# Performance work log

Hardware: AMD Instinct MI355X
Metric: run time of the kernel (lower is better)

Reference implementation:

```python
import jax, jax.numpy as jnp
import numpy as np

N = 100000
E = 1600000
EPS = 1e-5  # BatchNorm eps


def setup_inputs() -> dict:
    key = jax.random.key(0)
    ks = jax.random.split(key, 8)
    x = jax.random.normal(ks[0], (N, 8), jnp.float32)
    edge_index = jax.random.randint(ks[1], (2, E), 0, N, dtype=jnp.int64)

    def lin(k, i, o):
        return jax.random.normal(k, (i, o), jnp.float32) / np.float32(np.sqrt(i))

    d = {
        'x': x, 'edge_index': edge_index,
        'W1': lin(ks[2], 8, 64),  'b1': jnp.zeros((64,), jnp.float32),
        'g1': jnp.ones((64,), jnp.float32), 'be1': jnp.zeros((64,), jnp.float32),
        'rm1': jnp.zeros((64,), jnp.float32), 'rv1': jnp.ones((64,), jnp.float32),
        'W2': lin(ks[3], 64, 64), 'b2': jnp.zeros((64,), jnp.float32),
        'g2': jnp.ones((64,), jnp.float32), 'be2': jnp.zeros((64,), jnp.float32),
        'rm2': jnp.zeros((64,), jnp.float32), 'rv2': jnp.ones((64,), jnp.float32),
        'W3': lin(ks[4], 64, 32), 'b3': jnp.zeros((32,), jnp.float32),
        'g3': jnp.ones((32,), jnp.float32), 'be3': jnp.zeros((32,), jnp.float32),
        'rm3': jnp.zeros((32,), jnp.float32), 'rv3': jnp.ones((32,), jnp.float32),
        'Wc': lin(ks[5], 32, 2),  'bc': jnp.zeros((2,), jnp.float32),
    }
    return d


def _gcn_conv(x, W, b, src, dst):
    # PyG GCNConv (improved=False): add self-loops with weight 1, symmetric norm.
    h = x @ W                                               # [N, out]
    deg = jax.ops.segment_sum(jnp.ones((E,), x.dtype), dst, num_segments=N) + 1.0
    dinv = jax.lax.rsqrt(deg)                               # deg >= 1 (self loop)
    norm = dinv[src] * dinv[dst]                            # [E]
    agg = jax.ops.segment_sum(h[src] * norm[:, None], dst, num_segments=N)
    agg = agg + h * (dinv * dinv)[:, None]                  # self-loop messages
    return agg + b


def _bn_eval(x, g, be, rm, rv):
    return (x - rm) * jax.lax.rsqrt(rv + EPS) * g + be


def reference(x, edge_index,
              W1, b1, g1, be1, rm1, rv1,
              W2, b2, g2, be2, rm2, rv2,
              W3, b3, g3, be3, rm3, rv3,
              Wc, bc):
    src, dst = edge_index[0], edge_index[1]
    h = jax.nn.relu(_bn_eval(_gcn_conv(x, W1, b1, src, dst), g1, be1, rm1, rv1))
    h = jax.nn.relu(_bn_eval(_gcn_conv(h, W2, b2, src, dst), g2, be2, rm2, rv2))
    h = jax.nn.relu(_bn_eval(_gcn_conv(h, W3, b3, src, dst), g3, be3, rm3, rv3))
    logits = h @ Wc + bc                                    # [N, 2]
    return jax.nn.log_softmax(logits, axis=-1)
```

## Files before the change

### kernel.cpp

```cpp
#include <hip/hip_runtime.h>
#include <hip/hip_fp16.h>

#define BN_EPS 1e-5f
#define BCAP 5120
#define EDCAP_H64 768
#define EDCAP_CLS 1280

__device__ __forceinline__ unsigned f2u(float a, float b) {
  __half2 h = __floats2half2_rn(a, b);
  return *reinterpret_cast<unsigned*>(&h);
}
__device__ __forceinline__ __half2 uh2(unsigned u) {
  return *reinterpret_cast<__half2*>(&u);
}
__device__ __forceinline__ float2 h22f2(__half2 h) { return __half22float2(h); }
__device__ __forceinline__ __half2 h2shfl_xor(__half2 v, int m) {
  int i = *reinterpret_cast<int*>(&v);
  i = __shfl_xor(i, m);
  return *reinterpret_cast<__half2*>(&i);
}

__global__ void prep(const float* __restrict__ b1, const float* __restrict__ g1,
                     const float* __restrict__ be1, const float* __restrict__ rm1,
                     const float* __restrict__ rv1,
                     const float* __restrict__ b2, const float* __restrict__ g2,
                     const float* __restrict__ be2, const float* __restrict__ rm2,
                     const float* __restrict__ rv2,
                     const float* __restrict__ b3, const float* __restrict__ g3,
                     const float* __restrict__ be3, const float* __restrict__ rm3,
                     const float* __restrict__ rv3,
                     float* __restrict__ bn, int* __restrict__ bcur, int NB) {
  if (blockIdx.x == 0) {
    const int t = threadIdx.x;
    if (t < 64) {
      const float s = g1[t] * rsqrtf(rv1[t] + BN_EPS);
      bn[t] = s;
      bn[64 + t] = (b1[t] - rm1[t]) * s + be1[t];
    } else if (t < 128) {
      const int c = t - 64;
      const float s = g2[c] * rsqrtf(rv2[c] + BN_EPS);
      bn[128 + c] = s;
      bn[192 + c] = (b2[c] - rm2[c]) * s + be2[c];
    } else if (t < 160) {
      const int c = t - 128;
      const float s = g3[c] * rsqrtf(rv3[c] + BN_EPS);
      bn[256 + c] = s;
      bn[288 + c] = (b3[c] - rm3[c]) * s + be3[c];
    }
  } else {
    const int i = (blockIdx.x - 1) * 256 + threadIdx.x;
    if (i <= NB) bcur[i] = 0;
  }
}

__global__ void p1_partition(const int* __restrict__ ei, int* __restrict__ bucketbuf,
                             int* __restrict__ bcur, int E_, int NB) {
  __shared__ int pk[4096];
  __shared__ short bk[4096];
  __shared__ int hist[512];
  __shared__ int bbase[512];
  const int tid = threadIdx.x;
  const int e0 = blockIdx.x * 4096;
  const int ecount = min(4096, E_ - e0);
  for (int i = tid; i < NB; i += 256) hist[i] = 0;
  __syncthreads();
  for (int i = tid; i < ecount; i += 256) {
    const int s = ei[e0 + i];
    const int d = ei[(size_t)E_ + e0 + i];
    pk[i] = ((d & 255) << 24) | s;
    const int b = d >> 8;
    bk[i] = (short)b;
    atomicAdd(&hist[b], 1);
  }
  __syncthreads();
  for (int i = tid; i < NB; i += 256) {
    const int c = hist[i];
    bbase[i] = c ? atomicAdd(&bcur[i], c) : 0;
    hist[i] = 0;
  }
  __syncthreads();
  for (int i = tid; i < ecount; i += 256) {
    const int b = bk[i];
    const int slot = bbase[b] + atomicAdd(&hist[b], 1);
    bucketbuf[(size_t)b * BCAP + slot] = pk[i];
  }
}

__global__ void p2_sort(const int* __restrict__ bucketbuf, const int* __restrict__ bcur,
                        int* __restrict__ gcursor, int* __restrict__ edata,
                        int* __restrict__ rbeg, int* __restrict__ rend,
                        float* __restrict__ dinv, const float* __restrict__ x,
                        __half2* __restrict__ xs, int N_) {
  __shared__ int cntl[256];
  __shared__ int scn[256];
  __shared__ int cur[256];
  __shared__ float dinvl[256];
  __shared__ int sbuf[BCAP];
  __shared__ int sbase;
  const int b = blockIdx.x;
  const int tid = threadIdx.x;
  const int m = bcur[b];
  const int* srcp = bucketbuf + (size_t)b * BCAP;
  cntl[tid] = 0;
  __syncthreads();
  for (int i = tid; i < m; i += 256) atomicAdd(&cntl[(unsigned)srcp[i] >> 24], 1);
  __syncthreads();
  if (tid == 0) sbase = atomicAdd(gcursor, m);
  const int cnt = cntl[tid];
  scn[tid] = cnt;
  __syncthreads();
  for (int off = 1; off < 256; off <<= 1) {
    int u = (tid >= off) ? scn[tid - off] : 0;
    __syncthreads();
    scn[tid] += u;
    __syncthreads();
  }
  const int excl = scn[tid] - cnt;
  cur[tid] = excl;
  const int base = sbase;
  const int node = (b << 8) + tid;
  const float dn = rsqrtf((float)cnt + 1.0f);
  dinvl[tid] = dn;
  if (node < N_) {
    rbeg[node] = base + excl;
    rend[node] = base + excl + cnt;
    dinv[node] = dn;
  }
  __syncthreads();
  for (int i = tid; i < m; i += 256) {
    const int v = srcp[i];
    const int slot = atomicAdd(&cur[(unsigned)v >> 24], 1);
    sbuf[slot] = v & 0xFFFFFF;
  }
  __syncthreads();
  for (int i = tid; i < m; i += 256) edata[(size_t)base + i] = sbuf[i];
  const int nb0 = b << 8;
  for (int i = tid; i < 1024; i += 256) {
    const int nd = nb0 + (i >> 2);
    if (nd < N_) {
      const float d2 = dinvl[i >> 2];
      const float2 v2 = reinterpret_cast<const float2*>(x)[(size_t)nd * 4 + (i & 3)];
      xs[(size_t)nd * 4 + (i & 3)] = __floats2half2_rn(v2.x * d2, v2.y * d2);
    }
  }
}

__global__ void gx_mm1(const __half* __restrict__ xs, const float* __restrict__ dinv,
                       const int* __restrict__ rbeg, const int* __restrict__ rend,
                       const int* __restrict__ edata, const float* __restrict__ W1,
                       const float* __restrict__ bn, __half* __restrict__ t1, int n) {
  __shared__ float shagg[32][8];
  __shared__ float shw[8 * 64];
  const int tid = threadIdx.x;
  for (int i = tid; i < 512; i += 256) shw[i] = W1[i];
  const int node0 = blockIdx.x * 32;
  const int lane = tid & 63;
  const int nl = ((tid >> 6) << 3) + (lane >> 3);
  const int grp = lane & 7;
  const int node = node0 + nl;
  if (node < n) {
    const int beg = rbeg[node], end = rend[node];
    const uint4* xv = reinterpret_cast<const uint4*>(xs);
    __half2 c0 = __half2{0, 0}, c1 = c0, c2 = c0, c3 = c0;
    int e = beg + grp;
    for (; e + 8 < end; e += 16) {
      const uint4 q0 = xv[edata[e]];
      const uint4 q1 = xv[edata[e + 8]];
      c0 = __hadd2(c0, uh2(q0.x)); c1 = __hadd2(c1, uh2(q0.y));
      c2 = __hadd2(c2, uh2(q0.z)); c3 = __hadd2(c3, uh2(q0.w));
      c0 = __hadd2(c0, uh2(q1.x)); c1 = __hadd2(c1, uh2(q1.y));
      c2 = __hadd2(c2, uh2(q1.z)); c3 = __hadd2(c3, uh2(q1.w));
    }
    if (e < end) {
      const uint4 q = xv[edata[e]];
      c0 = __hadd2(c0, uh2(q.x)); c1 = __hadd2(c1, uh2(q.y));
      c2 = __hadd2(c2, uh2(q.z)); c3 = __hadd2(c3, uh2(q.w));
    }
#pragma unroll
    for (int m = 1; m <= 4; m <<= 1) {
      c0 = __hadd2(c0, h2shfl_xor(c0, m));
      c1 = __hadd2(c1, h2shfl_xor(c1, m));
      c2 = __hadd2(c2, h2shfl_xor(c2, m));
      c3 = __hadd2(c3, h2shfl_xor(c3, m));
    }
    if (grp == 0) {
      const uint4 q = xv[node];
      c0 = __hadd2(c0, uh2(q.x)); c1 = __hadd2(c1, uh2(q.y));
      c2 = __hadd2(c2, uh2(q.z)); c3 = __hadd2(c3, uh2(q.w));
      const float dn = dinv[node];
      const float2 f0 = h22f2(c0), f1 = h22f2(c1);
      const float2 f2 = h22f2(c2), f3 = h22f2(c3);
      shagg[nl][0] = f0.x * dn; shagg[nl][1] = f0.y * dn;
      shagg[nl][2] = f1.x * dn; shagg[nl][3] = f1.y * dn;
      shagg[nl][4] = f2.x * dn; shagg[nl][5] = f2.y * dn;
      shagg[nl][6] = f3.x * dn; shagg[nl][7] = f3.y * dn;
    }
  }
  __syncthreads();
  const int mn = tid >> 3;
  const int node2 = node0 + mn;
  if (node2 >= n) return;
  const int c = (tid & 7) * 8;
  float a[8] = {0, 0, 0, 0, 0, 0, 0, 0};
#pragma unroll
  for (int k = 0; k < 8; ++k) {
    const float s = shagg[mn][k];
#pragma unroll
    for (int j = 0; j < 8; ++j) a[j] += s * shw[k * 64 + c + j];
  }
  float v[8];
#pragma unroll
  for (int j = 0; j < 8; ++j) {
    float t = a[j] * bn[c + j] + bn[64 + c + j];
    v[j] = t > 0.0f ? t : 0.0f;
  }
  uint4 o;
  o.x = f2u(v[0], v[1]);
  o.y = f2u(v[2], v[3]);
  o.z = f2u(v[4], v[5]);
  o.w = f2u(v[6], v[7]);
  reinterpret_cast<uint4*>(t1)[(size_t)node2 * 8 + (tid & 7)] = o;
}

__global__ void mm2(const __half* __restrict__ t1, const float* __restrict__ W2,
                    const float* __restrict__ dinv, __half* __restrict__ h2, int n) {
  __shared__ __half2 shin[64 * 33];
  __shared__ uint4 shw[32 * 16];
  const int tid = threadIdx.x;
  const int node0 = blockIdx.x * 64;
  const __half2* t1h = reinterpret_cast<const __half2*>(t1);
  for (int i = tid; i < 64 * 32; i += 256) {
    const int nd = i >> 5, kp = i & 31;
    __half2 v = __half2{0, 0};
    if (node0 + nd < n) v = t1h[(size_t)(node0 + nd) * 32 + kp];
    shin[nd * 33 + kp] = v;
  }
  __half2* shwh = reinterpret_cast<__half2*>(shw);
  for (int i = tid; i < 32 * 64; i += 256) {
    const int kp = i >> 6, c = i & 63;
    shwh[kp * 64 + c] = __floats2half2_rn(W2[(2 * kp) * 64 + c], W2[(2 * kp + 1) * 64 + c]);
  }
  __syncthreads();

  const int cq = tid & 15;
  const int nb = (tid >> 4) * 4;
  float acc[4][4];
#pragma unroll
  for (int j = 0; j < 4; ++j)
#pragma unroll
    for (int k = 0; k < 4; ++k) acc[j][k] = 0.0f;

  for (int kp = 0; kp < 32; ++kp) {
    const uint4 wq = shw[kp * 16 + cq];
    const float2 w0 = h22f2(uh2(wq.x)), w1 = h22f2(uh2(wq.y));
    const float2 w2 = h22f2(uh2(wq.z)), w3 = h22f2(uh2(wq.w));
#pragma unroll
    for (int j = 0; j < 4; ++j) {
      const float2 s = h22f2(shin[(nb + j) * 33 + kp]);
      acc[j][0] += s.x * w0.x + s.y * w0.y;
      acc[j][1] += s.x * w1.x + s.y * w1.y;
      acc[j][2] += s.x * w2.x + s.y * w2.y;
      acc[j][3] += s.x * w3.x + s.y * w3.y;
    }
  }
#pragma unroll
  for (int j = 0; j < 4; ++j) {
    const int node = node0 + nb + j;
    if (node < n) {
      const float dn = dinv[node];
      uint2 o;
      o.x = f2u(acc[j][0] * dn, acc[j][1] * dn);
      o.y = f2u(acc[j][2] * dn, acc[j][3] * dn);
      reinterpret_cast<uint2*>(h2)[(size_t)node * 16 + cq] = o;
    }
  }
}

__global__ void gather_h64(const __half* __restrict__ h, const float* __restrict__ dinv,
                           const int* __restrict__ rbeg, const int* __restrict__ rend,
                           const int* __restrict__ edata, __half* __restrict__ agg, int n) {
  __shared__ int se[EDCAP_H64];
  const int tid = threadIdx.x;
  const int node0 = blockIdx.x * 8;
  const int last = min(node0 + 7, n - 1);
  const int gb = rbeg[node0];
  const int total = rend[last] - gb;
  const bool lds = (total <= EDCAP_H64);
  if (lds) {
    for (int i = tid; i < total; i += 256) se[i] = edata[gb + i];
  }
  __syncthreads();
  const int lane = tid & 63;
  const int node = node0 + ((tid >> 6) << 1) + (lane >> 5);
  if (node >= n) return;
  const int sub = lane & 31;
  const int qi = sub & 7;
  const int grp = sub >> 3;
  const uint4* hv = reinterpret_cast<const uint4*>(h);
  __half2 c0 = __half2{0, 0}, c1 = c0, c2 = c0, c3 = c0;
  if (lds) {
    const int beg = rbeg[node] - gb, end = rend[node] - gb;
    int e = beg + grp;
    for (; e + 12 < end; e += 16) {
      const int s0 = se[e], s1 = se[e + 4], s2 = se[e + 8], s3 = se[e + 12];
      const uint4 q0 = hv[(size_t)s0 * 8 + qi];
      const uint4 q1 = hv[(size_t)s1 * 8 + qi];
      const uint4 q2 = hv[(size_t)s2 * 8 + qi];
      const uint4 q3 = hv[(size_t)s3 * 8 + qi];
      c0 = __hadd2(c0, uh2(q0.x)); c1 = __hadd2(c1, uh2(q0.y));
      c2 = __hadd2(c2, uh2(q0.z)); c3 = __hadd2(c3, uh2(q0.w));
      c0 = __hadd2(c0, uh2(q1.x)); c1 = __hadd2(c1, uh2(q1.y));
      c2 = __hadd2(c2, uh2(q1.z)); c3 = __hadd2(c3, uh2(q1.w));
      c0 = __hadd2(c0, uh2(q2.x)); c1 = __hadd2(c1, uh2(q2.y));
      c2 = __hadd2(c2, uh2(q2.z)); c3 = __hadd2(c3, uh2(q2.w));
      c0 = __hadd2(c0, uh2(q3.x)); c1 = __hadd2(c1, uh2(q3.y));
      c2 = __hadd2(c2, uh2(q3.z)); c3 = __hadd2(c3, uh2(q3.w));
    }
    for (; e < end; e += 4) {
      const uint4 q = hv[(size_t)se[e] * 8 + qi];
      c0 = __hadd2(c0, uh2(q.x)); c1 = __hadd2(c1, uh2(q.y));
      c2 = __hadd2(c2, uh2(q.z)); c3 = __hadd2(c3, uh2(q.w));
    }
  } else {
    const int beg = rbeg[node], end = rend[node];
    int e = beg + grp;
    for (; e + 12 < end; e += 16) {
      const int s0 = edata[e], s1 = edata[e + 4], s2 = edata[e + 8], s3 = edata[e + 12];
      const uint4 q0 = hv[(size_t)s0 * 8 + qi];
      const uint4 q1 = hv[(size_t)s1 * 8 + qi];
      const uint4 q2 = hv[(size_t)s2 * 8 + qi];
      const uint4 q3 = hv[(size_t)s3 * 8 + qi];
      c0 = __hadd2(c0, uh2(q0.x)); c1 = __hadd2(c1, uh2(q0.y));
      c2 = __hadd2(c2, uh2(q0.z)); c3 = __hadd2(c3, uh2(q0.w));
      c0 = __hadd2(c0, uh2(q1.x)); c1 = __hadd2(c1, uh2(q1.y));
      c2 = __hadd2(c2, uh2(q1.z)); c3 = __hadd2(c3, uh2(q1.w));
      c0 = __hadd2(c0, uh2(q2.x)); c1 = __hadd2(c1, uh2(q2.y));
      c2 = __hadd2(c2, uh2(q2.z)); c3 = __hadd2(c3, uh2(q2.w));
      c0 = __hadd2(c0, uh2(q3.x)); c1 = __hadd2(c1, uh2(q3.y));
      c2 = __hadd2(c2, uh2(q3.z)); c3 = __hadd2(c3, uh2(q3.w));
    }
    for (; e < end; e += 4) {
      const uint4 q = hv[(size_t)edata[e] * 8 + qi];
      c0 = __hadd2(c0, uh2(q.x)); c1 = __hadd2(c1, uh2(q.y));
      c2 = __hadd2(c2, uh2(q.z)); c3 = __hadd2(c3, uh2(q.w));
    }
  }
#pragma unroll
  for (int m = 8; m <= 16; m <<= 1) {
    c0 = __hadd2(c0, h2shfl_xor(c0, m));
    c1 = __hadd2(c1, h2shfl_xor(c1, m));
    c2 = __hadd2(c2, h2shfl_xor(c2, m));
    c3 = __hadd2(c3, h2shfl_xor(c3, m));
  }
  if (grp == 0) {
    const uint4 q = hv[(size_t)node * 8 + qi];
    c0 = __hadd2(c0, uh2(q.x)); c1 = __hadd2(c1, uh2(q.y));
    c2 = __hadd2(c2, uh2(q.z)); c3 = __hadd2(c3, uh2(q.w));
    const float dn = dinv[node];
    const float2 f0 = h22f2(c0), f1 = h22f2(c1);
    const float2 f2 = h22f2(c2), f3 = h22f2(c3);
    uint4 o;
    o.x = f2u(f0.x * dn, f0.y * dn);
    o.y = f2u(f1.x * dn, f1.y * dn);
    o.z = f2u(f2.x * dn, f2.y * dn);
    o.w = f2u(f3.x * dn, f3.y * dn);
    reinterpret_cast<uint4*>(agg)[(size_t)node * 8 + qi] = o;
  }
}

__global__ void mm3_act(const __half* __restrict__ agg2, const float* __restrict__ W3,
                        const float* __restrict__ bn, const float* __restrict__ dinv,
                        __half* __restrict__ h3, int n) {
  __shared__ __half2 shin[128 * 33];
  __shared__ uint4 shw[32 * 8];
  const int tid = threadIdx.x;
  const int node0 = blockIdx.x * 128;
  const __half2* ah = reinterpret_cast<const __half2*>(agg2);
  for (int i = tid; i < 128 * 32; i += 256) {
    const int nd = i >> 5, kp = i & 31;
    __half2 o = __half2{0, 0};
    if (node0 + nd < n) {
      const float2 v = h22f2(ah[(size_t)(node0 + nd) * 32 + kp]);
      float v0 = v.x * bn[128 + 2 * kp] + bn[192 + 2 * kp];
      float v1 = v.y * bn[128 + 2 * kp + 1] + bn[192 + 2 * kp + 1];
      v0 = v0 > 0.0f ? v0 : 0.0f;
      v1 = v1 > 0.0f ? v1 : 0.0f;
      o = __floats2half2_rn(v0, v1);
    }
    shin[nd * 33 + kp] = o;
  }
  __half2* shwh = reinterpret_cast<__half2*>(shw);
  for (int i = tid; i < 32 * 32; i += 256) {
    const int kp = i >> 5, c = i & 31;
    shwh[kp * 32 + c] = __floats2half2_rn(W3[(2 * kp) * 32 + c], W3[(2 * kp + 1) * 32 + c]);
  }
  __syncthreads();

  const int cq = tid & 7;
  const int nb = (tid >> 3) * 4;
  float acc[4][4];
#pragma unroll
  for (int j = 0; j < 4; ++j)
#pragma unroll
    for (int k = 0; k < 4; ++k) acc[j][k] = 0.0f;

  for (int kp = 0; kp < 32; ++kp) {
    const uint4 wq = shw[kp * 8 + cq];
    const float2 w0 = h22f2(uh2(wq.x)), w1 = h22f2(uh2(wq.y));
    const float2 w2 = h22f2(uh2(wq.z)), w3 = h22f2(uh2(wq.w));
#pragma unroll
    for (int j = 0; j < 4; ++j) {
      const float2 s = h22f2(shin[(nb + j) * 33 + kp]);
      acc[j][0] += s.x * w0.x + s.y * w0.y;
      acc[j][1] += s.x * w1.x + s.y * w1.y;
      acc[j][2] += s.x * w2.x + s.y * w2.y;
      acc[j][3] += s.x * w3.x + s.y * w3.y;
    }
  }
#pragma unroll
  for (int j = 0; j < 4; ++j) {
    const int node = node0 + nb + j;
    if (node < n) {
      const float dn = dinv[node];
      uint2 o;
      o.x = f2u(acc[j][0] * dn, acc[j][1] * dn);
      o.y = f2u(acc[j][2] * dn, acc[j][3] * dn);
      reinterpret_cast<uint2*>(h3)[(size_t)node * 8 + cq] = o;
    }
  }
}

__global__ void gather_cls(const __half* __restrict__ h, const float* __restrict__ dinv,
                           const int* __restrict__ rbeg, const int* __restrict__ rend,
                           const int* __restrict__ edata, const float* __restrict__ bn,
                           const float* __restrict__ Wc, const float* __restrict__ bc,
                           float* __restrict__ out, int n) {
  __shared__ int se[EDCAP_CLS];
  const int tid = threadIdx.x;
  const int node0 = blockIdx.x * 16;
  const int last = min(node0 + 15, n - 1);
  const int gb = rbeg[node0];
  const int total = rend[last] - gb;
  const bool lds = (total <= EDCAP_CLS);
  if (lds) {
    for (int i = tid; i < total; i += 256) se[i] = edata[gb + i];
  }
  __syncthreads();
  const int lane = tid & 63;
  const int node = node0 + ((tid >> 6) << 2) + (lane >> 4);
  if (node >= n) return;
  const int qi = lane & 3;
  const int grp = (lane >> 2) & 3;
  const uint4* hv = reinterpret_cast<const uint4*>(h);
  __half2 c0 = __half2{0, 0}, c1 = c0, c2 = c0, c3 = c0;
  if (lds) {
    const int beg = rbeg[node] - gb, end = rend[node] - gb;
    int e = beg + grp;
    for (; e + 12 < end; e += 16) {
      const int s0 = se[e], s1 = se[e + 4], s2 = se[e + 8], s3 = se[e + 12];
      const uint4 q0 = hv[(size_t)s0 * 4 + qi];
      const uint4 q1 = hv[(size_t)s1 * 4 + qi];
      const uint4 q2 = hv[(size_t)s2 * 4 + qi];
      const uint4 q3 = hv[(size_t)s3 * 4 + qi];
      c0 = __hadd2(c0, uh2(q0.x)); c1 = __hadd2(c1, uh2(q0.y));
      c2 = __hadd2(c2, uh2(q0.z)); c3 = __hadd2(c3, uh2(q0.w));
      c0 = __hadd2(c0, uh2(q1.x)); c1 = __hadd2(c1, uh2(q1.y));
      c2 = __hadd2(c2, uh2(q1.z)); c3 = __hadd2(c3, uh2(q1.w));
      c0 = __hadd2(c0, uh2(q2.x)); c1 = __hadd2(c1, uh2(q2.y));
      c2 = __hadd2(c2, uh2(q2.z)); c3 = __hadd2(c3, uh2(q2.w));
      c0 = __hadd2(c0, uh2(q3.x)); c1 = __hadd2(c1, uh2(q3.y));
      c2 = __hadd2(c2, uh2(q3.z)); c3 = __hadd2(c3, uh2(q3.w));
    }
    for (; e < end; e += 4) {
      const uint4 q = hv[(size_t)se[e] * 4 + qi];
      c0 = __hadd2(c0, uh2(q.x)); c1 = __hadd2(c1, uh2(q.y));
      c2 = __hadd2(c2, uh2(q.z)); c3 = __hadd2(c3, uh2(q.w));
    }
  } else {
    const int beg = rbeg[node], end = rend[node];
    int e = beg + grp;
    for (; e + 12 < end; e += 16) {
      const int s0 = edata[e], s1 = edata[e + 4], s2 = edata[e + 8], s3 = edata[e + 12];
      const uint4 q0 = hv[(size_t)s0 * 4 + qi];
      const uint4 q1 = hv[(size_t)s1 * 4 + qi];
      const uint4 q2 = hv[(size_t)s2 * 4 + qi];
      const uint4 q3 = hv[(size_t)s3 * 4 + qi];
      c0 = __hadd2(c0, uh2(q0.x)); c1 = __hadd2(c1, uh2(q0.y));
      c2 = __hadd2(c2, uh2(q0.z)); c3 = __hadd2(c3, uh2(q0.w));
      c0 = __hadd2(c0, uh2(q1.x)); c1 = __hadd2(c1, uh2(q1.y));
      c2 = __hadd2(c2, uh2(q1.z)); c3 = __hadd2(c3, uh2(q1.w));
      c0 = __hadd2(c0, uh2(q2.x)); c1 = __hadd2(c1, uh2(q2.y));
      c2 = __hadd2(c2, uh2(q2.z)); c3 = __hadd2(c3, uh2(q2.w));
      c0 = __hadd2(c0, uh2(q3.x)); c1 = __hadd2(c1, uh2(q3.y));
      c2 = __hadd2(c2, uh2(q3.z)); c3 = __hadd2(c3, uh2(q3.w));
    }
    for (; e < end; e += 4) {
      const uint4 q = hv[(size_t)edata[e] * 4 + qi];
      c0 = __hadd2(c0, uh2(q.x)); c1 = __hadd2(c1, uh2(q.y));
      c2 = __hadd2(c2, uh2(q.z)); c3 = __hadd2(c3, uh2(q.w));
    }
  }
#pragma unroll
  for (int m = 4; m <= 8; m <<= 1) {
    c0 = __hadd2(c0, h2shfl_xor(c0, m));
    c1 = __hadd2(c1, h2shfl_xor(c1, m));
    c2 = __hadd2(c2, h2shfl_xor(c2, m));
    c3 = __hadd2(c3, h2shfl_xor(c3, m));
  }
  if (grp != 0) return;
  {
    const uint4 q = hv[(size_t)node * 4 + qi];
    c0 = __hadd2(c0, uh2(q.x)); c1 = __hadd2(c1, uh2(q.y));
    c2 = __hadd2(c2, uh2(q.z)); c3 = __hadd2(c3, uh2(q.w));
  }
  const float dn = dinv[node];
  const float2 f0 = h22f2(c0), f1 = h22f2(c1);
  const float2 f2 = h22f2(c2), f3 = h22f2(c3);
  const float v[8] = {f0.x * dn, f0.y * dn, f1.x * dn, f1.y * dn,
                      f2.x * dn, f2.y * dn, f3.x * dn, f3.y * dn};
  float l0 = 0.0f, l1 = 0.0f;
#pragma unroll
  for (int j = 0; j < 8; ++j) {
    const int c = qi * 8 + j;
    float t = v[j] * bn[256 + c] + bn[288 + c];
    t = t > 0.0f ? t : 0.0f;
    const float2 w = *reinterpret_cast<const float2*>(&Wc[c * 2]);
    l0 += t * w.x;
    l1 += t * w.y;
  }
  l0 += __shfl_xor(l0, 1); l1 += __shfl_xor(l1, 1);
  l0 += __shfl_xor(l0, 2); l1 += __shfl_xor(l1, 2);
  if (qi == 0) {
    l0 += bc[0];
    l1 += bc[1];
    const float m = fmaxf(l0, l1);
    const float lse = m + log1pf(expf(-fabsf(l0 - l1)));
    *reinterpret_cast<float2*>(&out[(size_t)node * 2]) = make_float2(l0 - lse, l1 - lse);
  }
}

extern "C" void kernel_launch(void* const* d_in, const int* in_sizes, int n_in,
                              void* d_out, int out_size, void* d_ws, size_t ws_size,
                              hipStream_t stream) {
  const float* x  = (const float*)d_in[0];
  const int* ei   = (const int*)d_in[1];
  const float* W1 = (const float*)d_in[2];
  const float* b1 = (const float*)d_in[3];
  const float* g1 = (const float*)d_in[4];
  const float* be1 = (const float*)d_in[5];
  const float* rm1 = (const float*)d_in[6];
  const float* rv1 = (const float*)d_in[7];
  const float* W2 = (const float*)d_in[8];
  const float* b2 = (const float*)d_in[9];
  const float* g2 = (const float*)d_in[10];
  const float* be2 = (const float*)d_in[11];
  const float* rm2 = (const float*)d_in[12];
  const float* rv2 = (const float*)d_in[13];
  const float* W3 = (const float*)d_in[14];
  const float* b3 = (const float*)d_in[15];
  const float* g3 = (const float*)d_in[16];
  const float* be3 = (const float*)d_in[17];
  const float* rm3 = (const float*)d_in[18];
  const float* rv3 = (const float*)d_in[19];
  const float* Wc = (const float*)d_in[20];
  const float* bc = (const float*)d_in[21];

  const int N_ = in_sizes[0] / 8;
  const int E_ = in_sizes[1] / 2;
  const int NB = (N_ + 255) >> 8;

  auto align = [](size_t v) { return (v + 255) & ~(size_t)255; };
  char* ws = (char*)d_ws;
  size_t off = 0;
  float* dinv   = (float*)(ws + off); off += align((size_t)N_ * 4);
  int* bcur     = (int*)(ws + off);   off += align(((size_t)NB + 1) * 4);
  int* rbeg     = (int*)(ws + off);   off += align((size_t)N_ * 4);
  int* rend     = (int*)(ws + off);   off += align((size_t)N_ * 4);
  float* bnbuf  = (float*)(ws + off); off += align(320 * 4);
  int* edata    = (int*)(ws + off);   off += align((size_t)E_ * 4);
  __half* xs    = (__half*)(ws + off); off += align((size_t)N_ * 8 * 2);
  char* regionA = ws + off;           off += align((size_t)N_ * 64 * 2);
  char* regionB = ws + off;           off += align((size_t)N_ * 64 * 2);

  int* bucketbuf = (int*)regionA;
  __half* t1   = (__half*)regionA;
  __half* agg2 = (__half*)regionA;
  __half* h2   = (__half*)regionB;
  __half* h3   = (__half*)regionB;
  int* gcursor = bcur + NB;

  prep<<<1 + (NB + 1 + 255) / 256, 256, 0, stream>>>(b1, g1, be1, rm1, rv1,
                                                     b2, g2, be2, rm2, rv2,
                                                     b3, g3, be3, rm3, rv3, bnbuf, bcur, NB);
  p1_partition<<<(E_ + 4095) / 4096, 256, 0, stream>>>(ei, bucketbuf, bcur, E_, NB);
  p2_sort<<<NB, 256, 0, stream>>>(bucketbuf, bcur, gcursor, edata, rbeg, rend,
                                  dinv, x, (__half2*)xs, N_);

  gx_mm1<<<(N_ + 31) / 32, 256, 0, stream>>>(xs, dinv, rbeg, rend, edata, W1, bnbuf, t1, N_);

  mm2<<<(N_ + 63) / 64, 256, 0, stream>>>(t1, W2, dinv, h2, N_);
  gather_h64<<<(N_ + 7) / 8, 256, 0, stream>>>(h2, dinv, rbeg, rend, edata, agg2, N_);

  mm3_act<<<(N_ + 127) / 128, 256, 0, stream>>>(agg2, W3, bnbuf, dinv, h3, N_);
  gather_cls<<<(N_ + 15) / 16, 256, 0, stream>>>(h3, dinv, rbeg, rend, edata,
                                                 bnbuf, Wc, bc, (float*)d_out, N_);
}
```

Before: 166.7 us.

## Fuse layer-1 aggregate with both dense matmuls and gather with mm3

Merges gx_mm1 and mm2 into one kernel that keeps the layer-1 activations in LDS and applies W2 directly. It also merges the layer-2 gather with BN/ReLU and the W3 matmul, so the 64-wide intermediate t1 and agg2 never go to global memory. This removes two kernel launches and two full N×64 half-precision round-trips. The cost is higher LDS use per block and W2/W3 staging repeated in every small block, especially in gh64_mm3 with only 8 nodes per block.

```diff
diff --git a/kernel.cpp b/kernel.cpp
--- a/kernel.cpp
+++ b/kernel.cpp
@@ -145,15 +145,25 @@
   }
 }
 
-__global__ void gx_mm1(const __half* __restrict__ xs, const float* __restrict__ dinv,
-                       const int* __restrict__ rbeg, const int* __restrict__ rend,
-                       const int* __restrict__ edata, const float* __restrict__ W1,
-                       const float* __restrict__ bn, __half* __restrict__ t1, int n) {
+__global__ void l12(const __half* __restrict__ xs, const float* __restrict__ dinv,
+                    const int* __restrict__ rbeg, const int* __restrict__ rend,
+                    const int* __restrict__ edata, const float* __restrict__ W1,
+                    const float* __restrict__ W2, const float* __restrict__ bn,
+                    __half* __restrict__ h2, int n) {
+  __shared__ float shw1[8 * 64];
   __shared__ float shagg[32][8];
-  __shared__ float shw[8 * 64];
+  __shared__ __half2 sht1[32 * 33];
+  __shared__ uint4 shw2[32 * 16];
   const int tid = threadIdx.x;
-  for (int i = tid; i < 512; i += 256) shw[i] = W1[i];
   const int node0 = blockIdx.x * 32;
+  for (int i = tid; i < 512; i += 256) shw1[i] = W1[i];
+  {
+    __half2* shw2h = reinterpret_cast<__half2*>(shw2);
+    for (int i = tid; i < 32 * 64; i += 256) {
+      const int kp = i >> 6, c = i & 63;
+      shw2h[kp * 64 + c] = __floats2half2_rn(W2[(2 * kp) * 64 + c], W2[(2 * kp + 1) * 64 + c]);
+    }
+  }
   const int lane = tid & 63;
   const int nl = ((tid >> 6) << 3) + (lane >> 3);
   const int grp = lane & 7;
@@ -197,66 +207,43 @@
     }
   }
   __syncthreads();
-  const int mn = tid >> 3;
-  const int node2 = node0 + mn;
-  if (node2 >= n) return;
-  const int c = (tid & 7) * 8;
-  float a[8] = {0, 0, 0, 0, 0, 0, 0, 0};
-#pragma unroll
-  for (int k = 0; k < 8; ++k) {
-    const float s = shagg[mn][k];
-#pragma unroll
-    for (int j = 0; j < 8; ++j) a[j] += s * shw[k * 64 + c + j];
-  }
-  float v[8];
-#pragma unroll
-  for (int j = 0; j < 8; ++j) {
-    float t = a[j] * bn[c + j] + bn[64 + c + j];
-    v[j] = t > 0.0f ? t : 0.0f;
-  }
-  uint4 o;
-  o.x = f2u(v[0], v[1]);
-  o.y = f2u(v[2], v[3]);
-  o.z = f2u(v[4], v[5]);
-  o.w = f2u(v[6], v[7]);
-  reinterpret_cast<uint4*>(t1)[(size_t)node2 * 8 + (tid & 7)] = o;
-}
-
-__global__ void mm2(const __half* __restrict__ t1, const float* __restrict__ W2,
-                    const float* __restrict__ dinv, __half* __restrict__ h2, int n) {
-  __shared__ __half2 shin[64 * 33];
-  __shared__ uint4 shw[32 * 16];
-  const int tid = threadIdx.x;
-  const int node0 = blockIdx.x * 64;
-  const __half2* t1h = reinterpret_cast<const __half2*>(t1);
-  for (int i = tid; i < 64 * 32; i += 256) {
-    const int nd = i >> 5, kp = i & 31;
-    __half2 v = __half2{0, 0};
-    if (node0 + nd < n) v = t1h[(size_t)(node0 + nd) * 32 + kp];
-    shin[nd * 33 + kp] = v;
-  }
-  __half2* shwh = reinterpret_cast<__half2*>(shw);
-  for (int i = tid; i < 32 * 64; i += 256) {
-    const int kp = i >> 6, c = i & 63;
-    shwh[kp * 64 + c] = __floats2half2_rn(W2[(2 * kp) * 64 + c], W2[(2 * kp + 1) * 64 + c]);
-  }
-  __syncthreads();
-
+  {
+    const int mn = tid >> 3;
+    const int c = (tid & 7) * 8;
+    if (node0 + mn < n) {
+      float a[8] = {0, 0, 0, 0, 0, 0, 0, 0};
+#pragma unroll
+      for (int k = 0; k < 8; ++k) {
+        const float s = shagg[mn][k];
+#pragma unroll
+        for (int j = 0; j < 8; ++j) a[j] += s * shw1[k * 64 + c + j];
+      }
+      float v[8];
+#pragma unroll
+      for (int j = 0; j < 8; ++j) {
+        float t = a[j] * bn[c + j] + bn[64 + c + j];
+        v[j] = t > 0.0f ? t : 0.0f;
+      }
+#pragma unroll
+      for (int j = 0; j < 4; ++j)
+        sht1[mn * 33 + (tid & 7) * 4 + j] = __floats2half2_rn(v[2 * j], v[2 * j + 1]);
+    }
+  }
+  __syncthreads();
   const int cq = tid & 15;
-  const int nb = (tid >> 4) * 4;
-  float acc[4][4];
-#pragma unroll
-  for (int j = 0; j < 4; ++j)
+  const int nbs = (tid >> 4) * 2;
+  float acc[2][4];
+#pragma unroll
+  for (int j = 0; j < 2; ++j)
 #pragma unroll
     for (int k = 0; k < 4; ++k) acc[j][k] = 0.0f;
-
   for (int kp = 0; kp < 32; ++kp) {
-    const uint4 wq = shw[kp * 16 + cq];
+    const uint4 wq = shw2[kp * 16 + cq];
     const float2 w0 = h22f2(uh2(wq.x)), w1 = h22f2(uh2(wq.y));
     const float2 w2 = h22f2(uh2(wq.z)), w3 = h22f2(uh2(wq.w));
 #pragma unroll
-    for (int j = 0; j < 4; ++j) {
-      const float2 s = h22f2(shin[(nb + j) * 33 + kp]);
+    for (int j = 0; j < 2; ++j) {
+      const float2 s = h22f2(sht1[(nbs + j) * 33 + kp]);
       acc[j][0] += s.x * w0.x + s.y * w0.y;
       acc[j][1] += s.x * w1.x + s.y * w1.y;
       acc[j][2] += s.x * w2.x + s.y * w2.y;
@@ -264,22 +251,26 @@
     }
   }
 #pragma unroll
-  for (int j = 0; j < 4; ++j) {
-    const int node = node0 + nb + j;
-    if (node < n) {
-      const float dn = dinv[node];
+  for (int j = 0; j < 2; ++j) {
+    const int nd = node0 + nbs + j;
+    if (nd < n) {
+      const float dn = dinv[nd];
       uint2 o;
       o.x = f2u(acc[j][0] * dn, acc[j][1] * dn);
       o.y = f2u(acc[j][2] * dn, acc[j][3] * dn);
-      reinterpret_cast<uint2*>(h2)[(size_t)node * 16 + cq] = o;
-    }
-  }
-}
-
-__global__ void gather_h64(const __half* __restrict__ h, const float* __restrict__ dinv,
-                           const int* __restrict__ rbeg, const int* __restrict__ rend,
-                           const int* __restrict__ edata, __half* __restrict__ agg, int n) {
+      reinterpret_cast<uint2*>(h2)[(size_t)nd * 16 + cq] = o;
+    }
+  }
+}
+
+__global__ void gh64_mm3(const __half* __restrict__ h, const float* __restrict__ dinv,
+                         const int* __restrict__ rbeg, const int* __restrict__ rend,
+                         const int* __restrict__ edata, const float* __restrict__ W3,
+                         const float* __restrict__ bn, __half* __restrict__ h3, int n) {
   __shared__ int se[EDCAP_H64];
+  __shared__ __half2 shagg2[8 * 33];
+  __shared__ __half2 shw3[32 * 32];
+  __shared__ float shbn[128];
   const int tid = threadIdx.x;
   const int node0 = blockIdx.x * 8;
   const int last = min(node0 + 7, n - 1);
@@ -289,144 +280,107 @@
   if (lds) {
     for (int i = tid; i < total; i += 256) se[i] = edata[gb + i];
   }
+  for (int i = tid; i < 32 * 32; i += 256) {
+    const int kp = i >> 5, c = i & 31;
+    shw3[kp * 32 + c] = __floats2half2_rn(W3[(2 * kp) * 32 + c], W3[(2 * kp + 1) * 32 + c]);
+  }
+  if (tid < 128) shbn[tid] = bn[128 + tid];
   __syncthreads();
   const int lane = tid & 63;
   const int node = node0 + ((tid >> 6) << 1) + (lane >> 5);
-  if (node >= n) return;
   const int sub = lane & 31;
   const int qi = sub & 7;
   const int grp = sub >> 3;
-  const uint4* hv = reinterpret_cast<const uint4*>(h);
-  __half2 c0 = __half2{0, 0}, c1 = c0, c2 = c0, c3 = c0;
-  if (lds) {
-    const int beg = rbeg[node] - gb, end = rend[node] - gb;
-    int e = beg + grp;
-    for (; e + 12 < end; e += 16) {
-      const int s0 = se[e], s1 = se[e + 4], s2 = se[e + 8], s3 = se[e + 12];
-      const uint4 q0 = hv[(size_t)s0 * 8 + qi];
-      const uint4 q1 = hv[(size_t)s1 * 8 + qi];
-      const uint4 q2 = hv[(size_t)s2 * 8 + qi];
-      const uint4 q3 = hv[(size_t)s3 * 8 + qi];
-      c0 = __hadd2(c0, uh2(q0.x)); c1 = __hadd2(c1, uh2(q0.y));
-      c2 = __hadd2(c2, uh2(q0.z)); c3 = __hadd2(c3, uh2(q0.w));
-      c0 = __hadd2(c0, uh2(q1.x)); c1 = __hadd2(c1, uh2(q1.y));
-      c2 = __hadd2(c2, uh2(q1.z)); c3 = __hadd2(c3, uh2(q1.w));
-      c0 = __hadd2(c0, uh2(q2.x)); c1 = __hadd2(c1, uh2(q2.y));
-      c2 = __hadd2(c2, uh2(q2.z)); c3 = __hadd2(c3, uh2(q2.w));
-      c0 = __hadd2(c0, uh2(q3.x)); c1 = __hadd2(c1, uh2(q3.y));
-      c2 = __hadd2(c2, uh2(q3.z)); c3 = __hadd2(c3, uh2(q3.w));
-    }
-    for (; e < end; e += 4) {
-      const uint4 q = hv[(size_t)se[e] * 8 + qi];
+  if (node < n) {
+    const uint4* hv = reinterpret_cast<const uint4*>(h);
+    __half2 c0 = __half2{0, 0}, c1 = c0, c2 = c0, c3 = c0;
+    if (lds) {
+      const int beg = rbeg[node] - gb, end = rend[node] - gb;
+      int e = beg + grp;
+      for (; e + 12 < end; e += 16) {
+        const int s0 = se[e], s1 = se[e + 4], s2 = se[e + 8], s3 = se[e + 12];
+        const uint4 q0 = hv[(size_t)s0 * 8 + qi];
+        const uint4 q1 = hv[(size_t)s1 * 8 + qi];
+        const uint4 q2 = hv[(size_t)s2 * 8 + qi];
+        const uint4 q3 = hv[(size_t)s3 * 8 + qi];
+        c0 = __hadd2(c0, uh2(q0.x)); c1 = __hadd2(c1, uh2(q0.y));
+        c2 = __hadd2(c2, uh2(q0.z)); c3 = __hadd2(c3, uh2(q0.w));
+        c0 = __hadd2(c0, uh2(q1.x)); c1 = __hadd2(c1, uh2(q1.y));
+        c2 = __hadd2(c2, uh2(q1.z)); c3 = __hadd2(c3, uh2(q1.w));
+        c0 = __hadd2(c0, uh2(q2.x)); c1 = __hadd2(c1, uh2(q2.y));
+        c2 = __hadd2(c2, uh2(q2.z)); c3 = __hadd2(c3, uh2(q2.w));
+        c0 = __hadd2(c0, uh2(q3.x)); c1 = __hadd2(c1, uh2(q3.y));
+        c2 = __hadd2(c2, uh2(q3.z)); c3 = __hadd2(c3, uh2(q3.w));
+      }
+      for (; e < end; e += 4) {
+        const uint4 q = hv[(size_t)se[e] * 8 + qi];
+        c0 = __hadd2(c0, uh2(q.x)); c1 = __hadd2(c1, uh2(q.y));
+        c2 = __hadd2(c2, uh2(q.z)); c3 = __hadd2(c3, uh2(q.w));
+      }
+    } else {
+      const int beg = rbeg[node], end = rend[node];
+      int e = beg + grp;
+      for (; e + 12 < end; e += 16) {
+        const int s0 = edata[e], s1 = edata[e + 4], s2 = edata[e + 8], s3 = edata[e + 12];
+        const uint4 q0 = hv[(size_t)s0 * 8 + qi];
+        const uint4 q1 = hv[(size_t)s1 * 8 + qi];
+        const uint4 q2 = hv[(size_t)s2 * 8 + qi];
+        const uint4 q3 = hv[(size_t)s3 * 8 + qi];
+        c0 = __hadd2(c0, uh2(q0.x)); c1 = __hadd2(c1, uh2(q0.y));
+        c2 = __hadd2(c2, uh2(q0.z)); c3 = __hadd2(c3, uh2(q0.w));
+        c0 = __hadd2(c0, uh2(q1.x)); c1 = __hadd2(c1, uh2(q1.y));
+        c2 = __hadd2(c2, uh2(q1.z)); c3 = __hadd2(c3, uh2(q1.w));
+        c0 = __hadd2(c0, uh2(q2.x)); c1 = __hadd2(c1, uh2(q2.y));
+        c2 = __hadd2(c2, uh2(q2.z)); c3 = __hadd2(c3, uh2(q2.w));
+        c0 = __hadd2(c0, uh2(q3.x)); c1 = __hadd2(c1, uh2(q3.y));
+        c2 = __hadd2(c2, uh2(q3.z)); c3 = __hadd2(c3, uh2(q3.w));
+      }
+      for (; e < end; e += 4) {
+        const uint4 q = hv[(size_t)edata[e] * 8 + qi];
+        c0 = __hadd2(c0, uh2(q.x)); c1 = __hadd2(c1, uh2(q.y));
+        c2 = __hadd2(c2, uh2(q.z)); c3 = __hadd2(c3, uh2(q.w));
+      }
+    }
+#pragma unroll
+    for (int m = 8; m <= 16; m <<= 1) {
+      c0 = __hadd2(c0, h2shfl_xor(c0, m));
+      c1 = __hadd2(c1, h2shfl_xor(c1, m));
+      c2 = __hadd2(c2, h2shfl_xor(c2, m));
+      c3 = __hadd2(c3, h2shfl_xor(c3, m));
+    }
+    if (grp == 0) {
+      const uint4 q = hv[(size_t)node * 8 + qi];
       c0 = __hadd2(c0, uh2(q.x)); c1 = __hadd2(c1, uh2(q.y));
       c2 = __hadd2(c2, uh2(q.z)); c3 = __hadd2(c3, uh2(q.w));
-    }
-  } else {
-    const int beg = rbeg[node], end = rend[node];
-    int e = beg + grp;
-    for (; e + 12 < end; e += 16) {
-      const int s0 = edata[e], s1 = edata[e + 4], s2 = edata[e + 8], s3 = edata[e + 12];
-      const uint4 q0 = hv[(size_t)s0 * 8 + qi];
-      const uint4 q1 = hv[(size_t)s1 * 8 + qi];
-      const uint4 q2 = hv[(size_t)s2 * 8 + qi];
-      const uint4 q3 = hv[(size_t)s3 * 8 + qi];
-      c0 = __hadd2(c0, uh2(q0.x)); c1 = __hadd2(c1, uh2(q0.y));
-      c2 = __hadd2(c2, uh2(q0.z)); c3 = __hadd2(c3, uh2(q0.w));
-      c0 = __hadd2(c0, uh2(q1.x)); c1 = __hadd2(c1, uh2(q1.y));
-      c2 = __hadd2(c2, uh2(q1.z)); c3 = __hadd2(c3, uh2(q1.w));
-      c0 = __hadd2(c0, uh2(q2.x)); c1 = __hadd2(c1, uh2(q2.y));
-      c2 = __hadd2(c2, uh2(q2.z)); c3 = __hadd2(c3, uh2(q2.w));
-      c0 = __hadd2(c0, uh2(q3.x)); c1 = __hadd2(c1, uh2(q3.y));
-      c2 = __hadd2(c2, uh2(q3.z)); c3 = __hadd2(c3, uh2(q3.w));
-    }
-    for (; e < end; e += 4) {
-      const uint4 q = hv[(size_t)edata[e] * 8 + qi];
-      c0 = __hadd2(c0, uh2(q.x)); c1 = __hadd2(c1, uh2(q.y));
-      c2 = __hadd2(c2, uh2(q.z)); c3 = __hadd2(c3, uh2(q.w));
-    }
-  }
-#pragma unroll
-  for (int m = 8; m <= 16; m <<= 1) {
-    c0 = __hadd2(c0, h2shfl_xor(c0, m));
-    c1 = __hadd2(c1, h2shfl_xor(c1, m));
-    c2 = __hadd2(c2, h2shfl_xor(c2, m));
-    c3 = __hadd2(c3, h2shfl_xor(c3, m));
-  }
-  if (grp == 0) {
-    const uint4 q = hv[(size_t)node * 8 + qi];
-    c0 = __hadd2(c0, uh2(q.x)); c1 = __hadd2(c1, uh2(q.y));
-    c2 = __hadd2(c2, uh2(q.z)); c3 = __hadd2(c3, uh2(q.w));
-    const float dn = dinv[node];
-    const float2 f0 = h22f2(c0), f1 = h22f2(c1);
-    const float2 f2 = h22f2(c2), f3 = h22f2(c3);
-    uint4 o;
-    o.x = f2u(f0.x * dn, f0.y * dn);
-    o.y = f2u(f1.x * dn, f1.y * dn);
-    o.z = f2u(f2.x * dn, f2.y * dn);
-    o.w = f2u(f3.x * dn, f3.y * dn);
-    reinterpret_cast<uint4*>(agg)[(size_t)node * 8 + qi] = o;
-  }
-}
-
-__global__ void mm3_act(const __half* __restrict__ agg2, const float* __restrict__ W3,
-                        const float* __restrict__ bn, const float* __restrict__ dinv,
-                        __half* __restrict__ h3, int n) {
-  __shared__ __half2 shin[128 * 33];
-  __shared__ uint4 shw[32 * 8];
-  const int tid = threadIdx.x;
-  const int node0 = blockIdx.x * 128;
-  const __half2* ah = reinterpret_cast<const __half2*>(agg2);
-  for (int i = tid; i < 128 * 32; i += 256) {
-    const int nd = i >> 5, kp = i & 31;
-    __half2 o = __half2{0, 0};
-    if (node0 + nd < n) {
-      const float2 v = h22f2(ah[(size_t)(node0 + nd) * 32 + kp]);
-      float v0 = v.x * bn[128 + 2 * kp] + bn[192 + 2 * kp];
-      float v1 = v.y * bn[128 + 2 * kp + 1] + bn[192 + 2 * kp + 1];
-      v0 = v0 > 0.0f ? v0 : 0.0f;
-      v1 = v1 > 0.0f ? v1 : 0.0f;
-      o = __floats2half2_rn(v0, v1);
-    }
-    shin[nd * 33 + kp] = o;
-  }
-  __half2* shwh = reinterpret_cast<__half2*>(shw);
-  for (int i = tid; i < 32 * 32; i += 256) {
-    const int kp = i >> 5, c = i & 31;
-    shwh[kp * 32 + c] = __floats2half2_rn(W3[(2 * kp) * 32 + c], W3[(2 * kp + 1) * 32 + c]);
-  }
-  __syncthreads();
-
-  const int cq = tid & 7;
-  const int nb = (tid >> 3) * 4;
-  float acc[4][4];
-#pragma unroll
-  for (int j = 0; j < 4; ++j)
-#pragma unroll
-    for (int k = 0; k < 4; ++k) acc[j][k] = 0.0f;
-
+      const float dn = dinv[node];
+      const int nl = node - node0;
+      const float2 f[4] = {h22f2(c0), h22f2(c1), h22f2(c2), h22f2(c3)};
+#pragma unroll
+      for (int j = 0; j < 4; ++j) {
+        const int ch = qi * 8 + 2 * j;
+        float v0 = f[j].x * dn * shbn[ch] + shbn[64 + ch];
+        float v1 = f[j].y * dn * shbn[ch + 1] + shbn[64 + ch + 1];
+        v0 = v0 > 0.0f ? v0 : 0.0f;
+        v1 = v1 > 0.0f ? v1 : 0.0f;
+        shagg2[nl * 33 + qi * 4 + j] = __floats2half2_rn(v0, v1);
+      }
+    }
+  }
+  __syncthreads();
+  const int mnode = node0 + (tid >> 5);
+  const int c = tid & 31;
+  float acc = 0.0f;
+#pragma unroll 8
   for (int kp = 0; kp < 32; ++kp) {
-    const uint4 wq = shw[kp * 8 + cq];
-    const float2 w0 = h22f2(uh2(wq.x)), w1 = h22f2(uh2(wq.y));
-    const float2 w2 = h22f2(uh2(wq.z)), w3 = h22f2(uh2(wq.w));
-#pragma unroll
-    for (int j = 0; j < 4; ++j) {
-      const float2 s = h22f2(shin[(nb + j) * 33 + kp]);
-      acc[j][0] += s.x * w0.x + s.y * w0.y;
-      acc[j][1] += s.x * w1.x + s.y * w1.y;
-      acc[j][2] += s.x * w2.x + s.y * w2.y;
-      acc[j][3] += s.x * w3.x + s.y * w3.y;
-    }
-  }
-#pragma unroll
-  for (int j = 0; j < 4; ++j) {
-    const int node = node0 + nb + j;
-    if (node < n) {
-      const float dn = dinv[node];
-      uint2 o;
-      o.x = f2u(acc[j][0] * dn, acc[j][1] * dn);
-      o.y = f2u(acc[j][2] * dn, acc[j][3] * dn);
-      reinterpret_cast<uint2*>(h3)[(size_t)node * 8 + cq] = o;
-    }
+    const float2 s = h22f2(shagg2[(tid >> 5) * 33 + kp]);
+    const float2 w = h22f2(shw3[kp * 32 + c]);
+    acc += s.x * w.x + s.y * w.y;
+  }
+  float outv = 0.0f;
+  if (mnode < n) outv = acc * dinv[mnode];
+  const float partner = __shfl_xor(outv, 1);
+  if ((c & 1) == 0 && mnode < n) {
+    reinterpret_cast<unsigned*>(h3)[(size_t)mnode * 16 + (c >> 1)] = f2u(outv, partner);
   }
 }
 
@@ -579,14 +533,12 @@
   float* bnbuf  = (float*)(ws + off); off += align(320 * 4);
   int* edata    = (int*)(ws + off);   off += align((size_t)E_ * 4);
   __half* xs    = (__half*)(ws + off); off += align((size_t)N_ * 8 * 2);
-  char* regionA = ws + off;           off += align((size_t)N_ * 64 * 2);
+  char* regionA = ws + off;           off += align((size_t)NB * BCAP * 4);
   char* regionB = ws + off;           off += align((size_t)N_ * 64 * 2);
 
   int* bucketbuf = (int*)regionA;
-  __half* t1   = (__half*)regionA;
-  __half* agg2 = (__half*)regionA;
+  __half* h3   = (__half*)regionA;
   __half* h2   = (__half*)regionB;
-  __half* h3   = (__half*)regionB;
   int* gcursor = bcur + NB;
 
   prep<<<1 + (NB + 1 + 255) / 256, 256, 0, stream>>>(b1, g1, be1, rm1, rv1,
@@ -596,12 +548,10 @@
   p2_sort<<<NB, 256, 0, stream>>>(bucketbuf, bcur, gcursor, edata, rbeg, rend,
                                   dinv, x, (__half2*)xs, N_);
 
-  gx_mm1<<<(N_ + 31) / 32, 256, 0, stream>>>(xs, dinv, rbeg, rend, edata, W1, bnbuf, t1, N_);
-
-  mm2<<<(N_ + 63) / 64, 256, 0, stream>>>(t1, W2, dinv, h2, N_);
-  gather_h64<<<(N_ + 7) / 8, 256, 0, stream>>>(h2, dinv, rbeg, rend, edata, agg2, N_);
-
-  mm3_act<<<(N_ + 127) / 128, 256, 0, stream>>>(agg2, W3, bnbuf, dinv, h3, N_);
+  l12<<<(N_ + 31) / 32, 256, 0, stream>>>(xs, dinv, rbeg, rend, edata, W1, W2, bnbuf, h2, N_);
+
+  gh64_mm3<<<(N_ + 7) / 8, 256, 0, stream>>>(h2, dinv, rbeg, rend, edata, W3, bnbuf, h3, N_);
+
   gather_cls<<<(N_ + 15) / 16, 256, 0, stream>>>(h3, dinv, rbeg, rend, edata,
                                                  bnbuf, Wc, bc, (float*)d_out, N_);
 }
```

Result: faster. 156.3 us (-6.3%).
